# Performance work log

Hardware: AMD Instinct MI355X
Metric: run time of the kernel (lower is better)

## Reference

```python
import jax, jax.numpy as jnp
import numpy as np

TOKENS = 50257
DIMS = 1024
BATCH = 4
SEQ = 4096


def setup_inputs() -> dict:
    key = jax.random.key(0)
    k1, k2 = jax.random.split(key)
    x = jax.random.randint(k1, (BATCH, SEQ), 0, TOKENS, dtype=jnp.int64 if jax.config.jax_enable_x64 else jnp.int32)
    # nn.Linear(tokens, dims).weight has shape [dims, tokens]
    W = jax.random.normal(k2, (DIMS, TOKENS), dtype=jnp.float32) * (1.0 / np.sqrt(TOKENS))
    return {"x": x, "W": W}


def reference(x, W):
    # Original: out = one_hot(x, tokens) @ W.T  (Linear with no bias).
    # one_hot @ W.T is mathematically a row gather from W.T: out[b, s, :] = W[:, x[b, s]].
    # We compute the identical result without materializing the [B, S, tokens] one-hot.
    return jnp.take(W.T, x, axis=0)  # [B, S, dims]
```

## Files before the change

### kernel.cpp

```cpp
#include <hip/hip_runtime.h>


#define DIMS    1024
#define TOKENS  50257
#define WBITS   7
#define WSIZE   128
#define NW      ((TOKENS + WSIZE - 1) / WSIZE)
#define PAD     129
#define NMAX    16384

__global__ __launch_bounds__(1024) void sort_kernel(
    const int* __restrict__ x, int n,
    int* __restrict__ offs,
    unsigned int* __restrict__ sorted)
{
    __shared__ int xl[NMAX];
    __shared__ int bins[NW];
    __shared__ int scanbuf[512];
    __shared__ int cursor[NW];
    const int t = threadIdx.x;

    const bool fits = (n <= NMAX);
    if (fits) for (int i = t; i < n; i += 1024) xl[i] = x[i];
    if (t < NW) bins[t] = 0;
    __syncthreads();
    const int* xs = fits ? xl : x;

    for (int i = t; i < n; i += 1024)
        atomicAdd(&bins[xs[i] >> WBITS], 1);
    __syncthreads();

    if (t < 512) scanbuf[t] = (t < NW) ? bins[t] : 0;
    __syncthreads();
    for (int off = 1; off < 512; off <<= 1) {
        int u = 0;
        if (t < 512 && t >= off) u = scanbuf[t - off];
        __syncthreads();
        if (t < 512) scanbuf[t] += u;
        __syncthreads();
    }
    if (t < NW) {
        offs[t + 1] = scanbuf[t];
        cursor[t]   = scanbuf[t] - bins[t];
    }
    if (t == 0) offs[0] = 0;
    __syncthreads();

    for (int i = t; i < n; i += 1024) {
        int tok = xs[i];
        int p = atomicAdd(&cursor[tok >> WBITS], 1);
        sorted[p] = ((unsigned int)i << 16) | (unsigned int)tok;
    }
}

__global__ __launch_bounds__(512) void embed_main(
    const float* __restrict__ W,
    const int* __restrict__ offs,
    const unsigned int* __restrict__ sorted,
    float* __restrict__ out)
{
    __shared__ float tile[WSIZE * PAD];
    const int w     = blockIdx.x;
    const int dbase = blockIdx.y * WSIZE;
    const int t     = threadIdx.x;
    const int id0   = w << WBITS;

    const int beg = offs[w];
    const int nn  = offs[w + 1] - beg;

    const int c  = t & 127;
    const int r0 = t >> 7;
    const int id = id0 + c;
    if (id < TOKENS) {
        #pragma unroll
        for (int i = 0; i < 32; ++i) {
            int r = (i << 2) + r0;
            tile[r * PAD + c] = W[(size_t)(dbase + r) * TOKENS + id];
        }
    }
    __syncthreads();

    const int d  = t & 127;
    const int jo = t >> 7;
    for (int jb = 0; jb < nn; jb += 4) {
        int j = jb + jo;
        if (j < nn) {
            unsigned int v = sorted[beg + j];
            int p   = (int)(v >> 16);
            int col = (int)(v & 0xFFFFu) - id0;
            out[(size_t)p * DIMS + dbase + d] = tile[d * PAD + col];
        }
    }
}

extern "C" void kernel_launch(void* const* d_in, const int* in_sizes, int n_in,
                              void* d_out, int out_size, void* d_ws, size_t ws_size,
                              hipStream_t stream) {
    const int*   x = (const int*)d_in[0];
    const float* W = (const float*)d_in[1];
    float*     out = (float*)d_out;

    const int n = in_sizes[0];

    int* offs              = (int*)d_ws;
    unsigned int* sorted   = (unsigned int*)(offs + (NW + 1));

    sort_kernel<<<1, 1024, 0, stream>>>(x, n, offs, sorted);

    dim3 grid(NW, DIMS / WSIZE);
    embed_main<<<grid, 512, 0, stream>>>(W, offs, sorted, out);
}
```

Before: 325.0 us.

## Fuse token bucketing into the gather kernel and stage W tiles via direct-to-LDS loads

Drops the separate single-block sort kernel. Each gather block now scans the token ids itself in segments, collecting the tokens that fall in its 256-wide vocabulary window into an LDS list through LDS atomics. The W tile (64 dims × 256 tokens) is loaded with global_load_lds straight into shared memory, and outputs are written with nontemporal stores. This removes a serial single-block launch and its workspace round trip. In exchange, every block re-reads all of x from cache, and correctness depends on the async LDS loads having completed by the barrier.

```diff
diff --git a/kernel.cpp b/kernel.cpp
--- a/kernel.cpp
+++ b/kernel.cpp
@@ -3,93 +3,81 @@
 
 #define DIMS    1024
 #define TOKENS  50257
-#define WBITS   7
-#define WSIZE   128
+#define WBITS   8
+#define WSIZE   256
 #define NW      ((TOKENS + WSIZE - 1) / WSIZE)
-#define PAD     129
-#define NMAX    16384
+#define DCH     64
+#define PAD     257
+#define NSEG    3072
+#define NTHR    512
+#define MAXSEG  16
 
-__global__ __launch_bounds__(1024) void sort_kernel(
+__device__ __forceinline__ void load_lds4(const float* g, float* l) {
+    __builtin_amdgcn_global_load_lds(
+        (const __attribute__((address_space(1))) void*)g,
+        (__attribute__((address_space(3))) void*)l,
+        4, 0, 0);
+}
+
+__global__ __launch_bounds__(512) void embed_fused(
     const int* __restrict__ x, int n,
-    int* __restrict__ offs,
-    unsigned int* __restrict__ sorted)
+    const float* __restrict__ W,
+    float* __restrict__ out)
 {
-    __shared__ int xl[NMAX];
-    __shared__ int bins[NW];
-    __shared__ int scanbuf[512];
-    __shared__ int cursor[NW];
-    const int t = threadIdx.x;
+    __shared__ float tile[DCH * PAD];
+    __shared__ unsigned int list[NSEG];
+    __shared__ int cnts[MAXSEG];
 
-    const bool fits = (n <= NMAX);
-    if (fits) for (int i = t; i < n; i += 1024) xl[i] = x[i];
-    if (t < NW) bins[t] = 0;
-    __syncthreads();
-    const int* xs = fits ? xl : x;
+    const int w     = blockIdx.x;
+    const int dbase = blockIdx.y * DCH;
+    const int t     = threadIdx.x;
+    const int id0   = w << WBITS;
+    const int lane  = t & 63;
+    const int wid   = t >> 6;
 
-    for (int i = t; i < n; i += 1024)
-        atomicAdd(&bins[xs[i] >> WBITS], 1);
+    if (t < MAXSEG) cnts[t] = 0;
     __syncthreads();
 
-    if (t < 512) scanbuf[t] = (t < NW) ? bins[t] : 0;
-    __syncthreads();
-    for (int off = 1; off < 512; off <<= 1) {
-        int u = 0;
-        if (t < 512 && t >= off) u = scanbuf[t - off];
-        __syncthreads();
-        if (t < 512) scanbuf[t] += u;
-        __syncthreads();
-    }
-    if (t < NW) {
-        offs[t + 1] = scanbuf[t];
-        cursor[t]   = scanbuf[t] - bins[t];
-    }
-    if (t == 0) offs[0] = 0;
-    __syncthreads();
-
-    for (int i = t; i < n; i += 1024) {
-        int tok = xs[i];
-        int p = atomicAdd(&cursor[tok >> WBITS], 1);
-        sorted[p] = ((unsigned int)i << 16) | (unsigned int)tok;
-    }
-}
-
-__global__ __launch_bounds__(512) void embed_main(
-    const float* __restrict__ W,
-    const int* __restrict__ offs,
-    const unsigned int* __restrict__ sorted,
-    float* __restrict__ out)
-{
-    __shared__ float tile[WSIZE * PAD];
-    const int w     = blockIdx.x;
-    const int dbase = blockIdx.y * WSIZE;
-    const int t     = threadIdx.x;
-    const int id0   = w << WBITS;
-
-    const int beg = offs[w];
-    const int nn  = offs[w + 1] - beg;
-
-    const int c  = t & 127;
-    const int r0 = t >> 7;
-    const int id = id0 + c;
-    if (id < TOKENS) {
-        #pragma unroll
-        for (int i = 0; i < 32; ++i) {
-            int r = (i << 2) + r0;
-            tile[r * PAD + c] = W[(size_t)(dbase + r) * TOKENS + id];
+    {
+        const int q   = wid & 3;
+        const int r0  = wid >> 2;
+        const int idc = id0 + q * 64 + lane;
+        if (idc < TOKENS) {
+            const float* src = W + (size_t)(dbase + r0) * TOKENS + idc;
+            float*       dst = tile + r0 * PAD + q * 64 + lane;
+            #pragma unroll
+            for (int it = 0; it < DCH / 2; ++it) {
+                load_lds4(src, dst);
+                src += (size_t)2 * TOKENS;
+                dst += 2 * PAD;
+            }
         }
     }
-    __syncthreads();
 
-    const int d  = t & 127;
-    const int jo = t >> 7;
-    for (int jb = 0; jb < nn; jb += 4) {
-        int j = jb + jo;
-        if (j < nn) {
-            unsigned int v = sorted[beg + j];
-            int p   = (int)(v >> 16);
-            int col = (int)(v & 0xFFFFu) - id0;
-            out[(size_t)p * DIMS + dbase + d] = tile[d * PAD + col];
+    int si = 0;
+    for (int s0 = 0; s0 < n; s0 += NSEG, ++si) {
+        const int send = (s0 + NSEG < n) ? s0 + NSEG : n;
+        for (int i = s0 + t; i < send; i += NTHR) {
+            const int tok = x[i];
+            const unsigned int col = (unsigned int)(tok - id0);
+            if (col < WSIZE) {
+                const int idx = atomicAdd(&cnts[si], 1);
+                list[idx] = ((unsigned int)i << 8) | col;
+            }
         }
+        __syncthreads();
+        const int m = cnts[si];
+
+        const int d  = t & 63;
+        const int jo = t >> 6;
+        for (int jb = jo; jb < m; jb += 8) {
+            const unsigned int v = list[jb];
+            const int p   = (int)(v >> 8);
+            const int col = (int)(v & 255u);
+            const float val = tile[d * PAD + col];
+            __builtin_nontemporal_store(val, &out[(size_t)p * DIMS + dbase + d]);
+        }
+        __syncthreads();
     }
 }
 
@@ -102,11 +90,6 @@
 
     const int n = in_sizes[0];
 
-    int* offs              = (int*)d_ws;
-    unsigned int* sorted   = (unsigned int*)(offs + (NW + 1));
-
-    sort_kernel<<<1, 1024, 0, stream>>>(x, n, offs, sorted);
-
-    dim3 grid(NW, DIMS / WSIZE);
-    embed_main<<<grid, 512, 0, stream>>>(W, offs, sorted, out);
+    dim3 grid(NW, DIMS / DCH);
+    embed_fused<<<grid, NTHR, 0, stream>>>(x, n, W, out);
 }
```

Result: slower. 349.5 us (+7.5%).
